# Performance work log

Measured on AMD Instinct MI355X. Metric: run time of the kernel, lower is better.

## Reference

```python
import math
import jax, jax.numpy as jnp
import numpy as np

B, N, IN_DIM, EDGE_DIM, H, D = 2, 256, 256, 16, 8, 64
INNER = H * D

def setup_inputs() -> dict:
    key = jax.random.key(0)
    ks = jax.random.split(key, 12)
    s_in = 1.0 / math.sqrt(IN_DIM)
    s_e = 1.0 / math.sqrt(EDGE_DIM)
    return {
        "nodes": jax.random.normal(ks[0], (B, N, IN_DIM), jnp.float32),
        "edges": jax.random.normal(ks[1], (B, N, N, EDGE_DIM), jnp.float32),
        "adjacency": jax.random.randint(ks[2], (B, N, N), 0, 2).astype(jnp.float32),
        "Wq": jax.random.uniform(ks[3], (IN_DIM, INNER), jnp.float32, -s_in, s_in),
        "bq": jax.random.uniform(ks[4], (INNER,), jnp.float32, -s_in, s_in),
        "Wk": jax.random.uniform(ks[5], (IN_DIM, INNER), jnp.float32, -s_in, s_in),
        "bk": jax.random.uniform(ks[6], (INNER,), jnp.float32, -s_in, s_in),
        "Wv": jax.random.uniform(ks[7], (IN_DIM, INNER), jnp.float32, -s_in, s_in),
        "bv": jax.random.uniform(ks[8], (INNER,), jnp.float32, -s_in, s_in),
        "We": jax.random.uniform(ks[9], (EDGE_DIM, INNER), jnp.float32, -s_e, s_e),
        "be": jax.random.uniform(ks[10], (INNER,), jnp.float32, -s_e, s_e),
    }

def _heads(x, b, n):
    # (b, n, h*d) -> (b*h, n, d)
    return x.reshape(b, n, H, D).transpose(0, 2, 1, 3).reshape(b * H, n, D)

def reference(nodes, edges, adjacency, Wq, bq, Wk, bk, Wv, bv, We, be):
    b, n, _ = nodes.shape
    q = _heads(nodes @ Wq + bq, b, n)  # (b*h, n, d)
    k = _heads(nodes @ Wk + bk, b, n)
    v = _heads(nodes @ Wv + bv, b, n)
    # edge-conditioned keys/values: e is per-(i, j)
    e = (edges @ We + be).reshape(b, n, n, H, D).transpose(0, 3, 1, 2, 4).reshape(b * H, n, n, D)
    k = k[:, None, :, :] + e  # (b*h, n, n, d)
    v = v[:, None, :, :] + e
    sim = jnp.einsum('bid,bijd->bij', q, k) / math.sqrt(D)  # (b*h, n, n)
    adj = jnp.broadcast_to(adjacency[:, None, :, :], (b, H, n, n)).reshape(b * H, n, n)
    # faithful to the original custom softmax, including the [0] indexing:
    # torch.mean(x, -1, keepdim=True)[0] -> mean over last dim, then take batch slice 0
    means = jnp.mean(sim, axis=-1, keepdims=True)[0]  # (n, 1), broadcasts over b*h
    x_exp = jnp.exp(sim - means) * adj
    denom = jnp.sum(x_exp, axis=-1, keepdims=True)
    denom = jnp.where(denom == 0, 1.0, denom)
    attn = x_exp / denom
    out = jnp.einsum('bij,bijd->bid', attn, v)  # (b*h, n, d)
    # average=False: concat heads
    out = out.reshape(b, H, n, D).transpose(0, 2, 1, 3).reshape(b, n, H * D)
    return out
```

## Files before the change

kernel.cpp:

```cpp
#include <hip/hip_runtime.h>
#include <hip/hip_bf16.h>

#define BB 2
#define NN 256
#define IN_DIM 256
#define EDGE_DIM 16
#define HH 8
#define DD 64
#define INNER 512
#define BH (BB*HH)
#define II 8

__global__ __launch_bounds__(256, 4)
void proj_kernel(const float* __restrict__ nodes,
                 const float* __restrict__ Wq, const float* __restrict__ bq,
                 const float* __restrict__ Wk, const float* __restrict__ bk,
                 const float* __restrict__ Wv, const float* __restrict__ bv,
                 float* __restrict__ qf, float* __restrict__ kT,
                 float* __restrict__ vf) {
    const int z = blockIdx.z;
    const float* W; const float* bias; float* out; int mode;
    if (z == 0)      { W = Wq; bias = bq; out = qf; mode = 0; }
    else if (z == 1) { W = Wk; bias = bk; out = kT; mode = 1; }
    else             { W = Wv; bias = bv; out = vf; mode = 0; }

    const int tid = threadIdx.x;
    const int half = blockIdx.x;
    const int r0 = blockIdx.y * 4;

    __shared__ float4 nsh4[4][IN_DIM / 4];
    {
        int rr = tid >> 6, c4 = tid & 63;
        nsh4[rr][c4] = ((const float4*)nodes)[(r0 + rr) * (IN_DIM / 4) + c4];
    }
    __syncthreads();

    const int col = half * 256 + tid;
    float acc[4] = {0.f, 0.f, 0.f, 0.f};
#pragma unroll 4
    for (int kc = 0; kc < IN_DIM / 4; ++kc) {
        float4 n0 = nsh4[0][kc], n1 = nsh4[1][kc], n2 = nsh4[2][kc], n3 = nsh4[3][kc];
        float w0 = W[(kc * 4 + 0) * INNER + col];
        float w1 = W[(kc * 4 + 1) * INNER + col];
        float w2 = W[(kc * 4 + 2) * INNER + col];
        float w3 = W[(kc * 4 + 3) * INNER + col];
        acc[0] += n0.x * w0 + n0.y * w1 + n0.z * w2 + n0.w * w3;
        acc[1] += n1.x * w0 + n1.y * w1 + n1.z * w2 + n1.w * w3;
        acc[2] += n2.x * w0 + n2.y * w1 + n2.z * w2 + n2.w * w3;
        acc[3] += n3.x * w0 + n3.y * w1 + n3.z * w2 + n3.w * w3;
    }
    const float bv2 = bias[col];
    const int h = col >> 6, d = col & 63;
#pragma unroll
    for (int rr = 0; rr < 4; ++rr) {
        int r = r0 + rr;
        int b = r >> 8, n = r & 255;
        float val = acc[rr] + bv2;
        if (mode == 0)
            out[((b * HH + h) * NN + n) * DD + d] = val;
        else
            out[((b * HH + h) * DD + d) * NN + n] = val;
    }
}

__global__ void means_kernel(const float* __restrict__ q,
                             const float* __restrict__ kT,
                             const float* __restrict__ edges,
                             const float* __restrict__ We,
                             const float* __restrict__ be,
                             float* __restrict__ means) {
    const int i = blockIdx.x;
    const int tid = threadIdx.x;
    __shared__ float qsh[DD];
    __shared__ float tsh[EDGE_DIM + 1];
    __shared__ float wred[4];
    if (tid < DD) qsh[tid] = q[i * DD + tid];
    __syncthreads();
    if (tid < EDGE_DIM) {
        float s = 0.f;
        for (int d = 0; d < DD; ++d) s += qsh[d] * We[tid * INNER + d];
        tsh[tid] = s;
    } else if (tid == EDGE_DIM) {
        float s = 0.f;
        for (int d = 0; d < DD; ++d) s += qsh[d] * be[d];
        tsh[EDGE_DIM] = s;
    }
    __syncthreads();
    const int j = tid;
    float sim = 0.f;
    for (int d = 0; d < DD; ++d) sim += qsh[d] * kT[d * NN + j];
    float ed = 0.f;
    const float* erow = &edges[(i * NN + j) * EDGE_DIM];
#pragma unroll
    for (int c = 0; c < EDGE_DIM; ++c) ed += erow[c] * tsh[c];
    sim = (sim + ed + tsh[EDGE_DIM]) * 0.125f;
    float s = sim;
    for (int o = 32; o > 0; o >>= 1) s += __shfl_down(s, o, 64);
    if ((tid & 63) == 0) wred[tid >> 6] = s;
    __syncthreads();
    if (tid == 0) means[i] = (wred[0] + wred[1] + wred[2] + wred[3]) * (1.f / NN);
}

__global__ __launch_bounds__(256, 4)
void attn_kernel(const float* __restrict__ q,
                 const float* __restrict__ kT,
                 const float* __restrict__ v,
                 const float* __restrict__ edges,
                 const float* __restrict__ adj,
                 const float* __restrict__ We,
                 const float* __restrict__ be,
                 const float* __restrict__ means,
                 float* __restrict__ out) {
    const int blk = blockIdx.x;
    const int bh = blk >> 5;
    const int it = blk & 31;
    const int i0 = it * II;
    const int b = bh >> 3, h = bh & 7;
    const int tid = threadIdx.x;
    const int j = tid;

    __shared__ float qsh[II][DD];
    __shared__ float tsh[II][EDGE_DIM + 1];
    __shared__ float xsh[II][NN];
    __shared__ float red[4][II][DD];
    __shared__ float wred2[16][II][EDGE_DIM];
    __shared__ float wsh[II][EDGE_DIM];
    __shared__ float dred[II][4];
    __shared__ float msh[II];
    __shared__ float dinv[II];
    __shared__ float scoef_sh[II];

    for (int idx = tid; idx < II * DD; idx += 256) {
        int ii = idx >> 6, d = idx & 63;
        qsh[ii][d] = q[(bh * NN + i0 + ii) * DD + d];
    }
    if (tid < II) msh[tid] = means[i0 + tid];
    __syncthreads();

    if (tid < II * (EDGE_DIM + 1)) {
        int ii = tid / (EDGE_DIM + 1), c = tid % (EDGE_DIM + 1);
        float s = 0.f;
        if (c < EDGE_DIM) {
            for (int d = 0; d < DD; ++d) s += qsh[ii][d] * We[c * INNER + h * DD + d];
        } else {
            for (int d = 0; d < DD; ++d) s += qsh[ii][d] * be[h * DD + d];
        }
        tsh[ii][c] = s;
    }
    __syncthreads();

    float sim[II];
#pragma unroll
    for (int ii = 0; ii < II; ++ii) sim[ii] = 0.f;
    const float* kbase = &kT[bh * DD * NN];
    for (int d = 0; d < DD; ++d) {
        float kv = kbase[d * NN + j];
#pragma unroll
        for (int ii = 0; ii < II; ++ii) sim[ii] += qsh[ii][d] * kv;
    }

    const int w = tid >> 6;
#pragma unroll
    for (int ii = 0; ii < II; ++ii) {
        const float4* e4 = (const float4*)&edges[((b * NN + i0 + ii) * NN + j) * EDGE_DIM];
        float4 e0 = e4[0], e1 = e4[1], e2 = e4[2], e3 = e4[3];
        float ed = tsh[ii][EDGE_DIM];
        ed += e0.x * tsh[ii][0] + e0.y * tsh[ii][1] + e0.z * tsh[ii][2] + e0.w * tsh[ii][3];
        ed += e1.x * tsh[ii][4] + e1.y * tsh[ii][5] + e1.z * tsh[ii][6] + e1.w * tsh[ii][7];
        ed += e2.x * tsh[ii][8] + e2.y * tsh[ii][9] + e2.z * tsh[ii][10] + e2.w * tsh[ii][11];
        ed += e3.x * tsh[ii][12] + e3.y * tsh[ii][13] + e3.z * tsh[ii][14] + e3.w * tsh[ii][15];
        float s = (sim[ii] + ed) * 0.125f;
        float x = __expf(s - msh[ii]) * adj[(b * NN + i0 + ii) * NN + j];
        xsh[ii][j] = x;
        for (int o = 32; o > 0; o >>= 1) x += __shfl_down(x, o, 64);
        if ((tid & 63) == 0) dred[ii][w] = x;
    }
    __syncthreads();
    if (tid < II) {
        float denom = dred[tid][0] + dred[tid][1] + dred[tid][2] + dred[tid][3];
        scoef_sh[tid] = (denom == 0.f) ? 0.f : 1.f;
        dinv[tid] = (denom == 0.f) ? 1.f : 1.f / denom;
    }
    __syncthreads();

    {
        const int d = tid & 63, part = tid >> 6;
        float acc[II];
#pragma unroll
        for (int ii = 0; ii < II; ++ii) acc[ii] = 0.f;
        const float* vb = &v[(bh * NN + part * 64) * DD + d];
        for (int jj4 = 0; jj4 < 16; ++jj4) {
            float av0 = vb[(jj4 * 4 + 0) * DD];
            float av1 = vb[(jj4 * 4 + 1) * DD];
            float av2 = vb[(jj4 * 4 + 2) * DD];
            float av3 = vb[(jj4 * 4 + 3) * DD];
#pragma unroll
            for (int ii = 0; ii < II; ++ii) {
                float4 x4 = *(const float4*)&xsh[ii][part * 64 + jj4 * 4];
                acc[ii] += x4.x * av0 + x4.y * av1 + x4.z * av2 + x4.w * av3;
            }
        }
#pragma unroll
        for (int ii = 0; ii < II; ++ii) red[part][ii][d] = acc[ii];
    }
    {
        const int c = tid & 15, p = tid >> 4;
        float accw[II];
#pragma unroll
        for (int ii = 0; ii < II; ++ii) accw[ii] = 0.f;
        for (int jj = 0; jj < 16; ++jj) {
            int jr = p * 16 + jj;
#pragma unroll
            for (int ii = 0; ii < II; ++ii)
                accw[ii] += xsh[ii][jr] *
                            edges[((b * NN + i0 + ii) * NN + jr) * EDGE_DIM + c];
        }
#pragma unroll
        for (int ii = 0; ii < II; ++ii) wred2[p][ii][c] = accw[ii];
    }
    __syncthreads();
    if (tid < II * EDGE_DIM) {
        int ii = tid >> 4, c = tid & 15;
        float t = 0.f;
#pragma unroll
        for (int p = 0; p < 16; ++p) t += wred2[p][ii][c];
        wsh[ii][c] = t;
    }
    __syncthreads();

    for (int idx = tid; idx < II * DD; idx += 256) {
        int ii = idx >> 6, d = idx & 63;
        float o = red[0][ii][d] + red[1][ii][d] + red[2][ii][d] + red[3][ii][d];
#pragma unroll
        for (int c = 0; c < EDGE_DIM; ++c)
            o += wsh[ii][c] * We[c * INNER + h * DD + d];
        out[(b * NN + i0 + ii) * INNER + h * DD + d] =
            o * dinv[ii] + scoef_sh[ii] * be[h * DD + d];
    }
}

extern "C" void kernel_launch(void* const* d_in, const int* in_sizes, int n_in,
                              void* d_out, int out_size, void* d_ws, size_t ws_size,
                              hipStream_t stream) {
    const float* nodes = (const float*)d_in[0];
    const float* edges = (const float*)d_in[1];
    const float* adj   = (const float*)d_in[2];
    const float* Wq = (const float*)d_in[3];
    const float* bq = (const float*)d_in[4];
    const float* Wk = (const float*)d_in[5];
    const float* bk = (const float*)d_in[6];
    const float* Wv = (const float*)d_in[7];
    const float* bv = (const float*)d_in[8];
    const float* We = (const float*)d_in[9];
    const float* be = (const float*)d_in[10];
    float* out = (float*)d_out;

    float* qf = (float*)d_ws;
    float* kT = qf + BH * NN * DD;
    float* vf = kT + BH * NN * DD;
    float* means = vf + BH * NN * DD;

    hipLaunchKernelGGL(proj_kernel, dim3(2, 128, 3), dim3(256), 0, stream,
                       nodes, Wq, bq, Wk, bk, Wv, bv, qf, kT, vf);
    hipLaunchKernelGGL(means_kernel, dim3(NN), dim3(256), 0, stream,
                       qf, kT, edges, We, be, means);
    hipLaunchKernelGGL(attn_kernel, dim3(BH * (NN / II)), dim3(256), 0, stream,
                       qf, kT, vf, edges, adj, We, be, means, out);
}
```

Measured before the change: 125.0 us.

## Fuse projection, means and attention into one cooperative kernel with grid syncs

Merges the three launches into a single cooperative kernel of 512 blocks. A grid-stride loop runs the projection tiles, then a grid sync, then the attention phase. Row means are now computed by the bh==0 blocks from their own sim values instead of a separate means kernel that recomputed them, and a second grid sync publishes them before the softmax. This removes two launch gaps and the duplicated means pass, at the cost of grid-wide barriers and requiring all 512 blocks to be co-resident.

```diff
diff --git a/kernel.cpp b/kernel.cpp
--- a/kernel.cpp
+++ b/kernel.cpp
@@ -1,5 +1,8 @@
 #include <hip/hip_runtime.h>
 #include <hip/hip_bf16.h>
+#include <hip/hip_cooperative_groups.h>
+
+namespace cg = cooperative_groups;
 
 #define BB 2
 #define NN 256
@@ -12,113 +15,22 @@
 #define II 8
 
 __global__ __launch_bounds__(256, 4)
-void proj_kernel(const float* __restrict__ nodes,
-                 const float* __restrict__ Wq, const float* __restrict__ bq,
-                 const float* __restrict__ Wk, const float* __restrict__ bk,
-                 const float* __restrict__ Wv, const float* __restrict__ bv,
-                 float* __restrict__ qf, float* __restrict__ kT,
-                 float* __restrict__ vf) {
-    const int z = blockIdx.z;
-    const float* W; const float* bias; float* out; int mode;
-    if (z == 0)      { W = Wq; bias = bq; out = qf; mode = 0; }
-    else if (z == 1) { W = Wk; bias = bk; out = kT; mode = 1; }
-    else             { W = Wv; bias = bv; out = vf; mode = 0; }
-
+void fused_kernel(const float* __restrict__ nodes,
+                  const float* __restrict__ edges,
+                  const float* __restrict__ adj,
+                  const float* __restrict__ Wq, const float* __restrict__ bq,
+                  const float* __restrict__ Wk, const float* __restrict__ bk,
+                  const float* __restrict__ Wv, const float* __restrict__ bv,
+                  const float* __restrict__ We, const float* __restrict__ be,
+                  float* __restrict__ qf, float* __restrict__ kT,
+                  float* __restrict__ vf, float* __restrict__ means,
+                  float* __restrict__ out)
+{
+    cg::grid_group grid = cg::this_grid();
     const int tid = threadIdx.x;
-    const int half = blockIdx.x;
-    const int r0 = blockIdx.y * 4;
+    const int bid = blockIdx.x;
 
     __shared__ float4 nsh4[4][IN_DIM / 4];
-    {
-        int rr = tid >> 6, c4 = tid & 63;
-        nsh4[rr][c4] = ((const float4*)nodes)[(r0 + rr) * (IN_DIM / 4) + c4];
-    }
-    __syncthreads();
-
-    const int col = half * 256 + tid;
-    float acc[4] = {0.f, 0.f, 0.f, 0.f};
-#pragma unroll 4
-    for (int kc = 0; kc < IN_DIM / 4; ++kc) {
-        float4 n0 = nsh4[0][kc], n1 = nsh4[1][kc], n2 = nsh4[2][kc], n3 = nsh4[3][kc];
-        float w0 = W[(kc * 4 + 0) * INNER + col];
-        float w1 = W[(kc * 4 + 1) * INNER + col];
-        float w2 = W[(kc * 4 + 2) * INNER + col];
-        float w3 = W[(kc * 4 + 3) * INNER + col];
-        acc[0] += n0.x * w0 + n0.y * w1 + n0.z * w2 + n0.w * w3;
-        acc[1] += n1.x * w0 + n1.y * w1 + n1.z * w2 + n1.w * w3;
-        acc[2] += n2.x * w0 + n2.y * w1 + n2.z * w2 + n2.w * w3;
-        acc[3] += n3.x * w0 + n3.y * w1 + n3.z * w2 + n3.w * w3;
-    }
-    const float bv2 = bias[col];
-    const int h = col >> 6, d = col & 63;
-#pragma unroll
-    for (int rr = 0; rr < 4; ++rr) {
-        int r = r0 + rr;
-        int b = r >> 8, n = r & 255;
-        float val = acc[rr] + bv2;
-        if (mode == 0)
-            out[((b * HH + h) * NN + n) * DD + d] = val;
-        else
-            out[((b * HH + h) * DD + d) * NN + n] = val;
-    }
-}
-
-__global__ void means_kernel(const float* __restrict__ q,
-                             const float* __restrict__ kT,
-                             const float* __restrict__ edges,
-                             const float* __restrict__ We,
-                             const float* __restrict__ be,
-                             float* __restrict__ means) {
-    const int i = blockIdx.x;
-    const int tid = threadIdx.x;
-    __shared__ float qsh[DD];
-    __shared__ float tsh[EDGE_DIM + 1];
-    __shared__ float wred[4];
-    if (tid < DD) qsh[tid] = q[i * DD + tid];
-    __syncthreads();
-    if (tid < EDGE_DIM) {
-        float s = 0.f;
-        for (int d = 0; d < DD; ++d) s += qsh[d] * We[tid * INNER + d];
-        tsh[tid] = s;
-    } else if (tid == EDGE_DIM) {
-        float s = 0.f;
-        for (int d = 0; d < DD; ++d) s += qsh[d] * be[d];
-        tsh[EDGE_DIM] = s;
-    }
-    __syncthreads();
-    const int j = tid;
-    float sim = 0.f;
-    for (int d = 0; d < DD; ++d) sim += qsh[d] * kT[d * NN + j];
-    float ed = 0.f;
-    const float* erow = &edges[(i * NN + j) * EDGE_DIM];
-#pragma unroll
-    for (int c = 0; c < EDGE_DIM; ++c) ed += erow[c] * tsh[c];
-    sim = (sim + ed + tsh[EDGE_DIM]) * 0.125f;
-    float s = sim;
-    for (int o = 32; o > 0; o >>= 1) s += __shfl_down(s, o, 64);
-    if ((tid & 63) == 0) wred[tid >> 6] = s;
-    __syncthreads();
-    if (tid == 0) means[i] = (wred[0] + wred[1] + wred[2] + wred[3]) * (1.f / NN);
-}
-
-__global__ __launch_bounds__(256, 4)
-void attn_kernel(const float* __restrict__ q,
-                 const float* __restrict__ kT,
-                 const float* __restrict__ v,
-                 const float* __restrict__ edges,
-                 const float* __restrict__ adj,
-                 const float* __restrict__ We,
-                 const float* __restrict__ be,
-                 const float* __restrict__ means,
-                 float* __restrict__ out) {
-    const int blk = blockIdx.x;
-    const int bh = blk >> 5;
-    const int it = blk & 31;
-    const int i0 = it * II;
-    const int b = bh >> 3, h = bh & 7;
-    const int tid = threadIdx.x;
-    const int j = tid;
-
     __shared__ float qsh[II][DD];
     __shared__ float tsh[II][EDGE_DIM + 1];
     __shared__ float xsh[II][NN];
@@ -130,13 +42,64 @@
     __shared__ float dinv[II];
     __shared__ float scoef_sh[II];
 
+    for (int tile = bid; tile < 768; tile += 512) {
+        const int z = tile >> 8;
+        const int rem = tile & 255;
+        const int half = rem >> 7;
+        const int rt = rem & 127;
+        const float* W; const float* bias; float* o; int mode;
+        if (z == 0)      { W = Wq; bias = bq; o = qf; mode = 0; }
+        else if (z == 1) { W = Wk; bias = bk; o = kT; mode = 1; }
+        else             { W = Wv; bias = bv; o = vf; mode = 0; }
+        const int r0 = rt * 4;
+        {
+            int rr = tid >> 6, c4 = tid & 63;
+            nsh4[rr][c4] = ((const float4*)nodes)[(r0 + rr) * (IN_DIM / 4) + c4];
+        }
+        __syncthreads();
+        const int col = half * 256 + tid;
+        float acc[4] = {0.f, 0.f, 0.f, 0.f};
+#pragma unroll 4
+        for (int kc = 0; kc < IN_DIM / 4; ++kc) {
+            float4 n0 = nsh4[0][kc], n1 = nsh4[1][kc], n2 = nsh4[2][kc], n3 = nsh4[3][kc];
+            float w0 = W[(kc * 4 + 0) * INNER + col];
+            float w1 = W[(kc * 4 + 1) * INNER + col];
+            float w2 = W[(kc * 4 + 2) * INNER + col];
+            float w3 = W[(kc * 4 + 3) * INNER + col];
+            acc[0] += n0.x * w0 + n0.y * w1 + n0.z * w2 + n0.w * w3;
+            acc[1] += n1.x * w0 + n1.y * w1 + n1.z * w2 + n1.w * w3;
+            acc[2] += n2.x * w0 + n2.y * w1 + n2.z * w2 + n2.w * w3;
+            acc[3] += n3.x * w0 + n3.y * w1 + n3.z * w2 + n3.w * w3;
+        }
+        const float bv2 = bias[col];
+        const int h = col >> 6, d = col & 63;
+#pragma unroll
+        for (int rr = 0; rr < 4; ++rr) {
+            int r = r0 + rr;
+            int b = r >> 8, n = r & 255;
+            float val = acc[rr] + bv2;
+            if (mode == 0)
+                o[((b * HH + h) * NN + n) * DD + d] = val;
+            else
+                o[((b * HH + h) * DD + d) * NN + n] = val;
+        }
+        __syncthreads();
+    }
+
+    grid.sync();
+
+    const int bh = bid >> 5;
+    const int it = bid & 31;
+    const int i0 = it * II;
+    const int b = bh >> 3, h = bh & 7;
+    const int j = tid;
+    const int w = tid >> 6;
+
     for (int idx = tid; idx < II * DD; idx += 256) {
         int ii = idx >> 6, d = idx & 63;
-        qsh[ii][d] = q[(bh * NN + i0 + ii) * DD + d];
-    }
-    if (tid < II) msh[tid] = means[i0 + tid];
-    __syncthreads();
-
+        qsh[ii][d] = qf[(bh * NN + i0 + ii) * DD + d];
+    }
+    __syncthreads();
     if (tid < II * (EDGE_DIM + 1)) {
         int ii = tid / (EDGE_DIM + 1), c = tid % (EDGE_DIM + 1);
         float s = 0.f;
@@ -149,17 +112,15 @@
     }
     __syncthreads();
 
-    float sim[II];
-#pragma unroll
-    for (int ii = 0; ii < II; ++ii) sim[ii] = 0.f;
+    float sv[II];
+#pragma unroll
+    for (int ii = 0; ii < II; ++ii) sv[ii] = 0.f;
     const float* kbase = &kT[bh * DD * NN];
     for (int d = 0; d < DD; ++d) {
         float kv = kbase[d * NN + j];
 #pragma unroll
-        for (int ii = 0; ii < II; ++ii) sim[ii] += qsh[ii][d] * kv;
-    }
-
-    const int w = tid >> 6;
+        for (int ii = 0; ii < II; ++ii) sv[ii] += qsh[ii][d] * kv;
+    }
 #pragma unroll
     for (int ii = 0; ii < II; ++ii) {
         const float4* e4 = (const float4*)&edges[((b * NN + i0 + ii) * NN + j) * EDGE_DIM];
@@ -169,8 +130,29 @@
         ed += e1.x * tsh[ii][4] + e1.y * tsh[ii][5] + e1.z * tsh[ii][6] + e1.w * tsh[ii][7];
         ed += e2.x * tsh[ii][8] + e2.y * tsh[ii][9] + e2.z * tsh[ii][10] + e2.w * tsh[ii][11];
         ed += e3.x * tsh[ii][12] + e3.y * tsh[ii][13] + e3.z * tsh[ii][14] + e3.w * tsh[ii][15];
-        float s = (sim[ii] + ed) * 0.125f;
-        float x = __expf(s - msh[ii]) * adj[(b * NN + i0 + ii) * NN + j];
+        sv[ii] = (sv[ii] + ed) * 0.125f;
+    }
+    if (bh == 0) {
+#pragma unroll
+        for (int ii = 0; ii < II; ++ii) {
+            float s = sv[ii];
+            for (int o = 32; o > 0; o >>= 1) s += __shfl_down(s, o, 64);
+            if ((tid & 63) == 0) dred[ii][w] = s;
+        }
+        __syncthreads();
+        if (tid < II)
+            means[i0 + tid] =
+                (dred[tid][0] + dred[tid][1] + dred[tid][2] + dred[tid][3]) * (1.f / NN);
+    }
+
+    grid.sync();
+
+    if (tid < II) msh[tid] = means[i0 + tid];
+    __syncthreads();
+
+#pragma unroll
+    for (int ii = 0; ii < II; ++ii) {
+        float x = __expf(sv[ii] - msh[ii]) * adj[(b * NN + i0 + ii) * NN + j];
         xsh[ii][j] = x;
         for (int o = 32; o > 0; o >>= 1) x += __shfl_down(x, o, 64);
         if ((tid & 63) == 0) dred[ii][w] = x;
@@ -188,7 +170,7 @@
         float acc[II];
 #pragma unroll
         for (int ii = 0; ii < II; ++ii) acc[ii] = 0.f;
-        const float* vb = &v[(bh * NN + part * 64) * DD + d];
+        const float* vb = &vf[(bh * NN + part * 64) * DD + d];
         for (int jj4 = 0; jj4 < 16; ++jj4) {
             float av0 = vb[(jj4 * 4 + 0) * DD];
             float av1 = vb[(jj4 * 4 + 1) * DD];
@@ -260,10 +242,11 @@
     float* vf = kT + BH * NN * DD;
     float* means = vf + BH * NN * DD;
 
-    hipLaunchKernelGGL(proj_kernel, dim3(2, 128, 3), dim3(256), 0, stream,
-                       nodes, Wq, bq, Wk, bk, Wv, bv, qf, kT, vf);
-    hipLaunchKernelGGL(means_kernel, dim3(NN), dim3(256), 0, stream,
-                       qf, kT, edges, We, be, means);
-    hipLaunchKernelGGL(attn_kernel, dim3(BH * (NN / II)), dim3(256), 0, stream,
-                       qf, kT, vf, edges, adj, We, be, means, out);
+    void* args[] = { (void*)&nodes, (void*)&edges, (void*)&adj,
+                     (void*)&Wq, (void*)&bq, (void*)&Wk, (void*)&bk,
+                     (void*)&Wv, (void*)&bv, (void*)&We, (void*)&be,
+                     (void*)&qf, (void*)&kT, (void*)&vf, (void*)&means,
+                     (void*)&out };
+    hipLaunchCooperativeKernel((const void*)fused_kernel, dim3(512), dim3(256),
+                               args, 0, stream);
 }
```

Measured after the change: 272.2 us. +117.7%, slower.

## Fold mean computation into attention kernel via linearity, dropping means kernel

Applied to the files above, without the earlier changes.

Removes the separate means kernel. The row mean of sim is linear in k and e, so it is computed as q0·(mean k + be) + mean(edges)·(q0 We). The projection kernel writes per-block partial sums of k for batch 0 head 0, and each attention block reduces those partials and the edge rows to build the mean. This saves one launch and a full pass over batch-0 edges, but every attention block now redundantly reads batch-0 edge rows and reduces the k partials.

```diff
diff --git a/kernel.cpp b/kernel.cpp
--- a/kernel.cpp
+++ b/kernel.cpp
@@ -17,7 +17,7 @@
                  const float* __restrict__ Wk, const float* __restrict__ bk,
                  const float* __restrict__ Wv, const float* __restrict__ bv,
                  float* __restrict__ qf, float* __restrict__ kT,
-                 float* __restrict__ vf) {
+                 float* __restrict__ vf, float* __restrict__ kpart) {
     const int z = blockIdx.z;
     const float* W; const float* bias; float* out; int mode;
     if (z == 0)      { W = Wq; bias = bq; out = qf; mode = 0; }
@@ -61,44 +61,9 @@
         else
             out[((b * HH + h) * DD + d) * NN + n] = val;
     }
-}
-
-__global__ void means_kernel(const float* __restrict__ q,
-                             const float* __restrict__ kT,
-                             const float* __restrict__ edges,
-                             const float* __restrict__ We,
-                             const float* __restrict__ be,
-                             float* __restrict__ means) {
-    const int i = blockIdx.x;
-    const int tid = threadIdx.x;
-    __shared__ float qsh[DD];
-    __shared__ float tsh[EDGE_DIM + 1];
-    __shared__ float wred[4];
-    if (tid < DD) qsh[tid] = q[i * DD + tid];
-    __syncthreads();
-    if (tid < EDGE_DIM) {
-        float s = 0.f;
-        for (int d = 0; d < DD; ++d) s += qsh[d] * We[tid * INNER + d];
-        tsh[tid] = s;
-    } else if (tid == EDGE_DIM) {
-        float s = 0.f;
-        for (int d = 0; d < DD; ++d) s += qsh[d] * be[d];
-        tsh[EDGE_DIM] = s;
-    }
-    __syncthreads();
-    const int j = tid;
-    float sim = 0.f;
-    for (int d = 0; d < DD; ++d) sim += qsh[d] * kT[d * NN + j];
-    float ed = 0.f;
-    const float* erow = &edges[(i * NN + j) * EDGE_DIM];
-#pragma unroll
-    for (int c = 0; c < EDGE_DIM; ++c) ed += erow[c] * tsh[c];
-    sim = (sim + ed + tsh[EDGE_DIM]) * 0.125f;
-    float s = sim;
-    for (int o = 32; o > 0; o >>= 1) s += __shfl_down(s, o, 64);
-    if ((tid & 63) == 0) wred[tid >> 6] = s;
-    __syncthreads();
-    if (tid == 0) means[i] = (wred[0] + wred[1] + wred[2] + wred[3]) * (1.f / NN);
+    if (z == 1 && half == 0 && blockIdx.y < 64 && tid < 64) {
+        kpart[blockIdx.y * 64 + tid] = acc[0] + acc[1] + acc[2] + acc[3] + 4.f * bv2;
+    }
 }
 
 __global__ __launch_bounds__(256, 4)
@@ -109,7 +74,7 @@
                  const float* __restrict__ adj,
                  const float* __restrict__ We,
                  const float* __restrict__ be,
-                 const float* __restrict__ means,
+                 const float* __restrict__ kpart,
                  float* __restrict__ out) {
     const int blk = blockIdx.x;
     const int bh = blk >> 5;
@@ -118,9 +83,14 @@
     const int b = bh >> 3, h = bh & 7;
     const int tid = threadIdx.x;
     const int j = tid;
+    const int w = tid >> 6;
 
     __shared__ float qsh[II][DD];
+    __shared__ float q0sh[II][DD];
     __shared__ float tsh[II][EDGE_DIM + 1];
+    __shared__ float t0sh[II][EDGE_DIM];
+    __shared__ float esumsh[II][EDGE_DIM];
+    __shared__ float kss[DD];
     __shared__ float xsh[II][NN];
     __shared__ float red[4][II][DD];
     __shared__ float wred2[16][II][EDGE_DIM];
@@ -132,9 +102,15 @@
 
     for (int idx = tid; idx < II * DD; idx += 256) {
         int ii = idx >> 6, d = idx & 63;
-        qsh[ii][d] = q[(bh * NN + i0 + ii) * DD + d];
-    }
-    if (tid < II) msh[tid] = means[i0 + tid];
+        qsh[ii][d]  = q[(bh * NN + i0 + ii) * DD + d];
+        q0sh[ii][d] = q[(i0 + ii) * DD + d];
+    }
+    if (tid < DD) {
+        float s = 0.f;
+#pragma unroll 8
+        for (int y = 0; y < 64; ++y) s += kpart[y * 64 + tid];
+        kss[tid] = s * (1.f / 256.f);
+    }
     __syncthreads();
 
     if (tid < II * (EDGE_DIM + 1)) {
@@ -147,6 +123,44 @@
         }
         tsh[ii][c] = s;
     }
+    if (tid >= 128 && tid < 128 + II * EDGE_DIM) {
+        int t = tid - 128, ii = t >> 4, c = t & 15;
+        float s = 0.f;
+        for (int d = 0; d < DD; ++d) s += q0sh[ii][d] * We[c * INNER + d];
+        t0sh[ii][c] = s;
+    }
+    __syncthreads();
+
+    {
+        const int c = tid & 15, p = tid >> 4;
+        float accw[II];
+#pragma unroll
+        for (int ii = 0; ii < II; ++ii) accw[ii] = 0.f;
+        for (int jj = 0; jj < 16; ++jj) {
+            int jr = p * 16 + jj;
+#pragma unroll
+            for (int ii = 0; ii < II; ++ii)
+                accw[ii] += edges[((i0 + ii) * NN + jr) * EDGE_DIM + c];
+        }
+#pragma unroll
+        for (int ii = 0; ii < II; ++ii) wred2[p][ii][c] = accw[ii];
+    }
+    __syncthreads();
+    if (tid < II * EDGE_DIM) {
+        int ii = tid >> 4, c = tid & 15;
+        float t = 0.f;
+#pragma unroll
+        for (int p = 0; p < 16; ++p) t += wred2[p][ii][c];
+        esumsh[ii][c] = t * (1.f / 256.f);
+    }
+    __syncthreads();
+    if (tid < II) {
+        float s = 0.f;
+        for (int d = 0; d < DD; ++d) s += q0sh[tid][d] * (kss[d] + be[d]);
+#pragma unroll
+        for (int c = 0; c < EDGE_DIM; ++c) s += esumsh[tid][c] * t0sh[tid][c];
+        msh[tid] = s * 0.125f;
+    }
     __syncthreads();
 
     float sim[II];
@@ -159,7 +173,6 @@
         for (int ii = 0; ii < II; ++ii) sim[ii] += qsh[ii][d] * kv;
     }
 
-    const int w = tid >> 6;
 #pragma unroll
     for (int ii = 0; ii < II; ++ii) {
         const float4* e4 = (const float4*)&edges[((b * NN + i0 + ii) * NN + j) * EDGE_DIM];
@@ -258,12 +271,10 @@
     float* qf = (float*)d_ws;
     float* kT = qf + BH * NN * DD;
     float* vf = kT + BH * NN * DD;
-    float* means = vf + BH * NN * DD;
+    float* kpart = vf + BH * NN * DD;
 
     hipLaunchKernelGGL(proj_kernel, dim3(2, 128, 3), dim3(256), 0, stream,
-                       nodes, Wq, bq, Wk, bk, Wv, bv, qf, kT, vf);
-    hipLaunchKernelGGL(means_kernel, dim3(NN), dim3(256), 0, stream,
-                       qf, kT, edges, We, be, means);
+                       nodes, Wq, bq, Wk, bk, Wv, bv, qf, kT, vf, kpart);
     hipLaunchKernelGGL(attn_kernel, dim3(BH * (NN / II)), dim3(256), 0, stream,
-                       qf, kT, vf, edges, adj, We, be, means, out);
+                       qf, kT, vf, edges, adj, We, be, kpart, out);
 }
```

Measured after the change: 127.3 us. Within noise of the previous version (+1.8%).
